# Kernel optimization log

Measured on AMD Instinct MI355X. Metric: run time of the kernel, lower is better.

The kernel has to match this reference:

```python
import jax, jax.numpy as jnp
import numpy as np

NUM_HEADS = 8
NEG_INF = -1e30


def _within_bucket_rank(idx):
    # idx: [U] int32 bucket ids; returns occurrence count of each id among earlier positions
    U = idx.shape[0]
    order = jnp.argsort(idx, stable=True)
    sv = idx[order]
    pos = jnp.arange(U, dtype=jnp.int32)
    is_start = jnp.concatenate([jnp.ones((1,), bool), sv[1:] != sv[:-1]])
    start = jax.lax.cummax(jnp.where(is_start, pos, 0))
    rank = pos - start
    return jnp.zeros(U, jnp.int32).at[order].set(rank)


def setup_inputs() -> dict:
    key = jax.random.key(0)
    ks = jax.random.split(key, 10)
    B, U, G, E = 8, 16384, 64, 128
    lin = jnp.linspace(0.0, 1.0, G)
    gx, gy = jnp.meshgrid(lin, lin, indexing='ij')
    xc_on_grid = jnp.broadcast_to(jnp.stack([gx, gy], -1), (B, G, G, 2)).astype(jnp.float32)
    s = 0.02
    return {
        'xc_off_grid': jax.random.uniform(ks[0], (B, U, 2), jnp.float32),
        'xc_on_grid': xc_on_grid,
        'zc_off_grid': jax.random.normal(ks[1], (B, U, E), jnp.float32),
        'zc_on_grid': jax.random.normal(ks[2], (B, G, G, E), jnp.float32),
        'latents': jax.random.normal(ks[3], (G * G, E), jnp.float32),
        'fake_embedding': jax.random.normal(ks[4], (E,), jnp.float32),
        'Wq': jax.random.normal(ks[5], (E, E), jnp.float32) * s,
        'Wk': jax.random.normal(ks[6], (E, E), jnp.float32) * s,
        'Wv': jax.random.normal(ks[7], (E, E), jnp.float32) * s,
        'Wo': jax.random.normal(ks[8], (E, E), jnp.float32) * s,
        'ignore_on_grid': 0,
    }


def _bucketize(xc_off_grid, xc_on_grid):
    # returns nearest flat grid index per off-grid point, shape [B, U] int32
    B = xc_off_grid.shape[0]
    dims = xc_on_grid.shape[1:-1]
    S = int(np.prod(dims))
    grid_shape = jnp.asarray(dims, jnp.float32)
    x_on = xc_on_grid.reshape(B, S, -1)
    xmin = x_on.min(axis=(0, 1))
    xmax = x_on.max(axis=(0, 1))
    spacing = (xmax - xmin) / (grid_shape - 1.0)
    nm = jnp.floor((xc_off_grid - xmin + spacing / 2) / spacing)
    nm = jnp.clip(nm, 0.0, grid_shape - 1.0)
    # strides as in the original: flip(cumprod([1, *dims])[:-1])
    strides = np.flip(np.cumprod(np.concatenate([[1], np.asarray(dims)]))[:-1]).astype(np.float32)
    return (nm * jnp.asarray(strides)).sum(-1).astype(jnp.int32)


def _mhca(latents_q, kv, valid, Wq, Wk, Wv, Wo):
    # latents_q: [N,1,E], kv: [N,P,E], valid: [N,P] bool
    N, P, E = kv.shape
    H, Dh = NUM_HEADS, E // NUM_HEADS
    q = (latents_q @ Wq).reshape(N, 1, H, Dh)
    k = (kv @ Wk).reshape(N, P, H, Dh)
    v = (kv @ Wv).reshape(N, P, H, Dh)
    scores = jnp.einsum('nqhd,nkhd->nhqk', q, k) / jnp.sqrt(jnp.asarray(Dh, q.dtype))
    scores = jnp.where(valid[:, None, None, :], scores, NEG_INF)
    attn = jax.nn.softmax(scores, axis=-1)
    out = jnp.einsum('nhqk,nkhd->nqhd', attn, v).reshape(N, 1, E)
    return out @ Wo


def reference(xc_off_grid, xc_on_grid, zc_off_grid, zc_on_grid, latents, fake_embedding, Wq, Wk, Wv, Wo, ignore_on_grid):
    B, U, E = zc_off_grid.shape
    dims = xc_on_grid.shape[1:-1]
    S = int(np.prod(dims))
    z_on = zc_on_grid.reshape(B, S, E)

    nearest_idx = _bucketize(xc_off_grid, xc_on_grid)          # [B, U]
    cumcount = jax.vmap(_within_bucket_rank)(nearest_idx)       # [B, U]
    flat_seg = (nearest_idx + jnp.arange(B, dtype=jnp.int32)[:, None] * S).reshape(-1)
    counts = jax.ops.segment_sum(jnp.ones(B * U, jnp.int32), flat_seg, num_segments=B * S)
    max_patch = int(jax.device_get(counts.max())) + 1           # +1 slot for on-grid/fake token

    # ragged scatter of off-grid tokens into padded per-bucket buffer
    grid_stacked = jnp.zeros((B * S, max_patch, E), zc_off_grid.dtype)
    grid_stacked = grid_stacked.at[flat_seg, cumcount.reshape(-1)].set(zc_off_grid.reshape(B * U, E))
    if ignore_on_grid:
        last = jnp.broadcast_to(fake_embedding, (B * S, E))
    else:
        last = z_on.reshape(B * S, E)
    grid_stacked = grid_stacked.at[:, -1].set(last)

    slot = jnp.arange(max_patch)
    valid = (slot[None, :] < counts[:, None]) | (slot[None, :] == max_patch - 1)  # [B*S, P]

    lat = jnp.broadcast_to(latents[None], (B, S, E)).reshape(B * S, 1, E)
    zc = _mhca(lat, grid_stacked, valid, Wq, Wk, Wv, Wo)        # [B*S, 1, E]
    return zc.reshape(B, *dims, E)
```

## Files before the change

kernel.cpp:

```cpp
#include <hip/hip_runtime.h>
#include <hip/hip_bf16.h>
#include <math.h>

namespace {
constexpr int B_  = 8;
constexpr int U_  = 16384;
constexpr int S_  = 4096;
constexpr int E_  = 128;
constexpr int NTOK  = B_ * U_;
constexpr int NCELL = B_ * S_;
constexpr int CAP = 32;
constexpr int SWZ2 = 2 * 16384;
constexpr int ASZ  = 128 * 1024;
}

typedef __attribute__((ext_vector_type(8))) short bf16x8;
typedef __attribute__((ext_vector_type(4))) float f32x4;

__device__ inline unsigned short bf16rne(float x) {
  unsigned u = __float_as_uint(x);
  u = u + 0x7fffu + ((u >> 16) & 1u);
  return (unsigned short)(u >> 16);
}

__device__ inline float bf16tof(unsigned short h) {
  return __uint_as_float(((unsigned)h) << 16);
}

__device__ inline bf16x8 pack8(float4 a, float4 b) {
  union { __hip_bfloat162 h; unsigned int u; } q0, q1, q2, q3;
  q0.h = __float22bfloat162_rn(make_float2(a.x, a.y));
  q1.h = __float22bfloat162_rn(make_float2(a.z, a.w));
  q2.h = __float22bfloat162_rn(make_float2(b.x, b.y));
  q3.h = __float22bfloat162_rn(make_float2(b.z, b.w));
  union { unsigned int u[4]; bf16x8 v; } r;
  r.u[0] = q0.u; r.u[1] = q1.u; r.u[2] = q2.u; r.u[3] = q3.u;
  return r.v;
}

__global__ __launch_bounds__(1024, 4) void setup_kernel(
    const float* __restrict__ Wq, const float* __restrict__ Wk,
    const float* __restrict__ Wv, const float* __restrict__ Wo,
    const float* __restrict__ xc_off,
    unsigned short* __restrict__ Wsw,
    unsigned short* __restrict__ Ahi, unsigned short* __restrict__ Alo,
    int* __restrict__ cnt, int* __restrict__ sorted) {
  const int tid = threadIdx.x;

  if (blockIdx.x < 16) {
    const int n = tid;
    const int eg = n >> 6, h = (n >> 3) & 7, el = n & 7;
    const int e = eg * 8 + el;
    const float* wk = Wk + (size_t)e * 128 + h * 16;
    float wkv[16];
#pragma unroll
    for (int j = 0; j < 16; j += 4) {
      float4 t = *(const float4*)(wk + j);
      wkv[j] = t.x; wkv[j + 1] = t.y; wkv[j + 2] = t.z; wkv[j + 3] = t.w;
    }
    union { unsigned short s[8]; uint4 v; } rh, rl;
#pragma unroll
    for (int r = 0; r < 8; ++r) {
      const int k = (blockIdx.x << 3) + r;
      const float* wq = Wq + (size_t)k * 128 + h * 16;
      float acc = 0.f;
#pragma unroll
      for (int j = 0; j < 16; j += 4) {
        float4 t = *(const float4*)(wq + j);
        acc = fmaf(t.x, wkv[j], acc);
        acc = fmaf(t.y, wkv[j + 1], acc);
        acc = fmaf(t.z, wkv[j + 2], acc);
        acc = fmaf(t.w, wkv[j + 3], acc);
      }
      acc *= 0.25f;
      const unsigned short hh = bf16rne(acc);
      rh.s[r] = hh;
      rl.s[r] = bf16rne(acc - bf16tof(hh));
    }
    const size_t fo = ((size_t)blockIdx.x * 1024 + n) * 8;
    *(uint4*)(Ahi + fo) = rh.v;
    *(uint4*)(Alo + fo) = rl.v;
  } else {
    const int base = (blockIdx.x - 16) * 1024 + tid;
    const int stride = 240 * 1024;
    for (int i = base; i < SWZ2 + NTOK; i += stride) {
      if (i < SWZ2) {
        const int w = i >> 14, e = i & 16383;
        const int k = e >> 7, n = e & 127;
        const float* src = (w == 0) ? Wv : Wo;
        Wsw[w * 16384 + (((k >> 3) * 128 + n) << 3) + (k & 7)] = bf16rne(src[e]);
      } else {
        const int tok = i - SWZ2;
        const int b = tok >> 14;
        const float sp = 1.0f / 63.0f;
        const float half = sp * 0.5f;
        const float x0 = xc_off[(size_t)tok * 2 + 0];
        const float x1 = xc_off[(size_t)tok * 2 + 1];
        float n0 = floorf((x0 - 0.0f + half) / sp);
        float n1 = floorf((x1 - 0.0f + half) / sp);
        n0 = fminf(fmaxf(n0, 0.0f), 63.0f);
        n1 = fminf(fmaxf(n1, 0.0f), 63.0f);
        const int seg = b * S_ + (int)(n0 * 64.0f + n1);
        const int rank = atomicAdd(&cnt[seg], 1);
        if (rank < CAP) sorted[seg * CAP + rank] = tok;
      }
    }
  }
}

__global__ __launch_bounds__(512, 4) void qkt_gemm(
    const float* __restrict__ latents,
    const unsigned short* __restrict__ Ahi,
    const unsigned short* __restrict__ Alo,
    unsigned short* __restrict__ QKt) {
  const int tid = threadIdx.x;
  const int wave = tid >> 6, lane = tid & 63;
  const int c = lane & 15, g = lane >> 4;
  const int rb = blockIdx.x >> 1, cb = blockIdx.x & 1;
  const int wr = wave >> 2, wc = wave & 3;
  const int t0 = rb * 32 + wr * 16;
  const int n0 = cb * 512 + wc * 128;

  f32x4 acc[8];
#pragma unroll
  for (int i = 0; i < 8; ++i) acc[i] = {0.f, 0.f, 0.f, 0.f};

  const float* arow = latents + (size_t)(t0 + c) * E_ + g * 8;
#pragma unroll
  for (int ks = 0; ks < 4; ++ks) {
    float4 a0 = *(const float4*)(arow + ks * 32);
    float4 a1 = *(const float4*)(arow + ks * 32 + 4);
    bf16x8 af = pack8(a0, a1);
    const size_t kg = (size_t)(ks * 4 + g) * 1024;
#pragma unroll
    for (int nt = 0; nt < 8; ++nt) {
      const size_t fo = (kg + n0 + nt * 16 + c) * 8;
      acc[nt] = __builtin_amdgcn_mfma_f32_16x16x32_bf16(
          af, *(const bf16x8*)(Ahi + fo), acc[nt], 0, 0, 0);
      acc[nt] = __builtin_amdgcn_mfma_f32_16x16x32_bf16(
          af, *(const bf16x8*)(Alo + fo), acc[nt], 0, 0, 0);
    }
  }
#pragma unroll
  for (int nt = 0; nt < 8; ++nt)
#pragma unroll
    for (int r = 0; r < 4; ++r)
      QKt[(size_t)(t0 + g * 4 + r) * 1024 + n0 + nt * 16 + c] = bf16rne(acc[nt][r]);
}

__global__ __launch_bounds__(512, 4) void fused_cells(
    const float* __restrict__ zc_off, const float* __restrict__ zc_on,
    const float* __restrict__ fake, const int* __restrict__ ignore_flag,
    const unsigned short* __restrict__ Wv_sw,
    const unsigned short* __restrict__ Wo_sw,
    const unsigned short* __restrict__ QKt, const int* __restrict__ cnt,
    const int* __restrict__ sorted, float* __restrict__ out) {
  __shared__ __align__(16) unsigned short wv[16384];
  __shared__ __align__(16) float wbuf[8][8][24];
  const int tid = threadIdx.x;
  {
    const uint4* sv = (const uint4*)Wv_sw;
    uint4* dv = (uint4*)wv;
#pragma unroll
    for (int i = 0; i < 4; ++i) dv[i * 512 + tid] = sv[i * 512 + tid];
  }
  const int ign = *ignore_flag;
  __syncthreads();

  const int wave = tid >> 6, lane = tid & 63;
  const int c = lane & 15, g = lane >> 4;
  const int half = c >> 3;
  const int hwr  = g >> 1;
  const bf16x8* bv = (const bf16x8*)wv;

  const int slot = blockIdx.x * 8 + wave;
  const int cA = slot * 2, cB = cA + 1;
  const int sA = cA & (S_ - 1);
  const int nA = min(cnt[cA], CAP);
  const int nB = min(cnt[cB], CAP);
  const int cH = half ? cB : cA;
  const int nH = half ? nB : nA;
  const int baseH = cH * CAP;
  const bf16x8* bqk = (const bf16x8*)(QKt + (size_t)(sA + half) * 1024);

  float num_acc[8], den_acc[8];
#pragma unroll
  for (int i = 0; i < 8; ++i) { num_acc[i] = 0.f; den_acc[i] = 0.f; }

  const int chunks = max((nA + 8) >> 3, (nB + 8) >> 3);

  for (int ch = 0; ch < chunks; ++ch) {
    const int jj = ch * 8 + (c & 7);
    const float* arow;
    if (jj < nH)       arow = zc_off + (size_t)sorted[baseH + jj] * E_;
    else if (jj == nH) arow = ign ? fake : (zc_on + (size_t)cH * E_);
    else               arow = zc_on;
    arow += g * 8;

    bf16x8 af[4];
#pragma unroll
    for (int ks = 0; ks < 4; ++ks) {
      float4 a0 = *(const float4*)(arow + ks * 32);
      float4 a1 = *(const float4*)(arow + ks * 32 + 4);
      af[ks] = pack8(a0, a1);
    }

    f32x4 aS = {0.f, 0.f, 0.f, 0.f};
#pragma unroll
    for (int ks = 0; ks < 4; ++ks)
      aS = __builtin_amdgcn_mfma_f32_16x16x32_bf16(af[ks], bqk[(ks * 4 + g) * 8 + (c & 7)], aS, 0, 0, 0);

    if (hwr == half) {
      float4 w4;
#pragma unroll
      for (int r = 0; r < 4; ++r) {
        const int t = g * 4 + r;
        const int jt = ch * 8 + (t & 7);
        ((float*)&w4)[r] = (jt <= nH) ? __expf(aS[r]) : 0.f;
      }
      *(float4*)&wbuf[wave][c & 7][g * 4] = w4;
    }

#pragma unroll 2
    for (int h = 0; h < 8; ++h) {
      const float4 wr4 = *(const float4*)&wbuf[wave][h][g * 4];

      const int bo = g * 128 + c + h * 16;
      f32x4 aV = {0.f, 0.f, 0.f, 0.f};
#pragma unroll
      for (int ks = 0; ks < 4; ++ks)
        aV = __builtin_amdgcn_mfma_f32_16x16x32_bf16(af[ks], bv[bo + ks * 512], aV, 0, 0, 0);

      float sv = 0.f, sd;
      sv = fmaf(wr4.x, aV[0], sv);
      sv = fmaf(wr4.y, aV[1], sv);
      sv = fmaf(wr4.z, aV[2], sv);
      sv = fmaf(wr4.w, aV[3], sv);
      sd = wr4.x + wr4.y + wr4.z + wr4.w;
      num_acc[h] += sv;
      den_acc[h] += sd;
    }
  }

#pragma unroll
  for (int i = 0; i < 8; ++i) {
    num_acc[i] += __shfl_xor(num_acc[i], 16, 64);
    den_acc[i] += __shfl_xor(den_acc[i], 16, 64);
  }
  const int hb = (g & 1) * 4;

  bf16x8 wof[4];
#pragma unroll
  for (int ks = 0; ks < 4; ++ks)
    wof[ks] = *(const bf16x8*)(Wo_sw +
        ((size_t)((ks * 4 + g) * 128 + wave * 16 + c)) * 8);

  __syncthreads();
  float* obuf = (float*)wv;
  const int lrow = wave * 2 + hwr;
#pragma unroll
  for (int b = 0; b < 4; ++b) {
    const int h = hb + b;
    obuf[lrow * 132 + h * 16 + c] = num_acc[h] / den_acc[h];
  }
  __syncthreads();

  const float* nrow = obuf + c * 132 + g * 8;
  f32x4 acc2 = {0.f, 0.f, 0.f, 0.f};
#pragma unroll
  for (int ks = 0; ks < 4; ++ks) {
    float4 a0 = *(const float4*)(nrow + ks * 32);
    float4 a1 = *(const float4*)(nrow + ks * 32 + 4);
    acc2 = __builtin_amdgcn_mfma_f32_16x16x32_bf16(pack8(a0, a1), wof[ks], acc2, 0, 0, 0);
  }
  const int cell0 = blockIdx.x * 16;
#pragma unroll
  for (int r = 0; r < 4; ++r)
    out[(size_t)(cell0 + g * 4 + r) * E_ + wave * 16 + c] = acc2[r];
}

extern "C" void kernel_launch(void* const* d_in, const int* in_sizes, int n_in,
                              void* d_out, int out_size, void* d_ws, size_t ws_size,
                              hipStream_t stream) {
  const float* xc_off  = (const float*)d_in[0];
  const float* zc_off  = (const float*)d_in[2];
  const float* zc_on   = (const float*)d_in[3];
  const float* latents = (const float*)d_in[4];
  const float* fake    = (const float*)d_in[5];
  const float* Wq      = (const float*)d_in[6];
  const float* Wk      = (const float*)d_in[7];
  const float* Wv      = (const float*)d_in[8];
  const float* Wo      = (const float*)d_in[9];
  const int*   ignore  = (const int*)d_in[10];

  float* out = (float*)d_out;

  unsigned short* QKt = (unsigned short*)d_ws;
  unsigned short* Wsw = QKt + (size_t)S_ * 1024;
  int* cnt    = (int*)(Wsw + SWZ2);
  int* sorted = cnt + NCELL;
  unsigned short* Ahi = (unsigned short*)(sorted + NCELL * CAP);
  unsigned short* Alo = Ahi + ASZ;
  unsigned short* Wv_sw = Wsw;
  unsigned short* Wo_sw = Wsw + 16384;

  hipMemsetAsync(cnt, 0, NCELL * sizeof(int), stream);
  setup_kernel<<<256, 1024, 0, stream>>>(Wq, Wk, Wv, Wo, xc_off,
                                         Wsw, Ahi, Alo, cnt, sorted);
  qkt_gemm<<<256, 512, 0, stream>>>(latents, Ahi, Alo, QKt);
  fused_cells<<<2048, 512, 0, stream>>>(zc_off, zc_on, fake, ignore,
                                        Wv_sw, Wo_sw, QKt, cnt, sorted, out);
}
```

Baseline: 185.2 us.

## Shrink fused_cells blocks, read Wv from global, restructure chunk loop and output GEMM

The fused cell kernel now runs 256-thread blocks with four waves instead of 512 threads, and drops the 32KB shared-memory staging of Wv, reading its fragments straight from global memory (L2/L1) so more blocks can be resident. The chunk loop is reordered so the on-grid token sits in slot 7 of the first chunk, which saves a chunk for some cell counts. The sorted index is read unconditionally, which is why the sorted buffer is now zeroed with a larger memset. The output projection computes two N-tiles per wave over a half-empty 16-row tile, which wastes half of that MFMA work. It also adds a larger memset and repeated global reads of Wv in exchange for lower LDS use and higher occupancy.

```diff
diff --git a/kernel.cpp b/kernel.cpp
--- a/kernel.cpp
+++ b/kernel.cpp
@@ -148,36 +148,31 @@
       QKt[(size_t)(t0 + g * 4 + r) * 1024 + n0 + nt * 16 + c] = bf16rne(acc[nt][r]);
 }
 
-__global__ __launch_bounds__(512, 4) void fused_cells(
+__global__ __launch_bounds__(256, 8) void fused_cells(
     const float* __restrict__ zc_off, const float* __restrict__ zc_on,
     const float* __restrict__ fake, const int* __restrict__ ignore_flag,
     const unsigned short* __restrict__ Wv_sw,
     const unsigned short* __restrict__ Wo_sw,
     const unsigned short* __restrict__ QKt, const int* __restrict__ cnt,
     const int* __restrict__ sorted, float* __restrict__ out) {
-  __shared__ __align__(16) unsigned short wv[16384];
-  __shared__ __align__(16) float wbuf[8][8][24];
+  __shared__ __align__(16) float wbuf[4][8][24];
+  __shared__ __align__(16) float obuf[16 * 132];
   const int tid = threadIdx.x;
-  {
-    const uint4* sv = (const uint4*)Wv_sw;
-    uint4* dv = (uint4*)wv;
-#pragma unroll
-    for (int i = 0; i < 4; ++i) dv[i * 512 + tid] = sv[i * 512 + tid];
-  }
+  for (int i = 8 * 132 + tid; i < 16 * 132; i += 256) obuf[i] = 0.f;
   const int ign = *ignore_flag;
-  __syncthreads();
 
   const int wave = tid >> 6, lane = tid & 63;
   const int c = lane & 15, g = lane >> 4;
   const int half = c >> 3;
   const int hwr  = g >> 1;
-  const bf16x8* bv = (const bf16x8*)wv;
-
-  const int slot = blockIdx.x * 8 + wave;
+  const bf16x8* bv = (const bf16x8*)Wv_sw;
+
+  const int slot = blockIdx.x * 4 + wave;
   const int cA = slot * 2, cB = cA + 1;
   const int sA = cA & (S_ - 1);
-  const int nA = min(cnt[cA], CAP);
-  const int nB = min(cnt[cB], CAP);
+  const int2 cc = *(const int2*)(cnt + cA);
+  const int nA = min(cc.x, CAP);
+  const int nB = min(cc.y, CAP);
   const int cH = half ? cB : cA;
   const int nH = half ? nB : nA;
   const int baseH = cH * CAP;
@@ -187,14 +182,14 @@
 #pragma unroll
   for (int i = 0; i < 8; ++i) { num_acc[i] = 0.f; den_acc[i] = 0.f; }
 
-  const int chunks = max((nA + 8) >> 3, (nB + 8) >> 3);
-
-  for (int ch = 0; ch < chunks; ++ch) {
-    const int jj = ch * 8 + (c & 7);
-    const float* arow;
-    if (jj < nH)       arow = zc_off + (size_t)sorted[baseH + jj] * E_;
-    else if (jj == nH) arow = ign ? fake : (zc_on + (size_t)cH * E_);
-    else               arow = zc_on;
+  int ch = 0;
+  do {
+    const int s = c & 7;
+    const bool isOn = (ch == 0) & (s == 7);
+    const int jj = (ch == 0) ? s : 7 + (ch - 1) * 8 + s;
+    const int sidx = sorted[baseH + (isOn ? 0 : min(jj, CAP - 1))];
+    const float* arow = isOn ? (ign ? fake : zc_on + (size_t)cH * E_)
+                             : zc_off + (size_t)sidx * E_;
     arow += g * 8;
 
     bf16x8 af[4];
@@ -214,9 +209,10 @@
       float4 w4;
 #pragma unroll
       for (int r = 0; r < 4; ++r) {
-        const int t = g * 4 + r;
-        const int jt = ch * 8 + (t & 7);
-        ((float*)&w4)[r] = (jt <= nH) ? __expf(aS[r]) : 0.f;
+        const int sl = (g * 4 + r) & 7;
+        const bool von = (ch == 0) & (sl == 7);
+        const int tj = (ch == 0) ? sl : 7 + (ch - 1) * 8 + sl;
+        ((float*)&w4)[r] = (von | (tj < nH)) ? __expf(aS[r]) : 0.f;
       }
       *(float4*)&wbuf[wave][c & 7][g * 4] = w4;
     }
@@ -240,7 +236,7 @@
       num_acc[h] += sv;
       den_acc[h] += sd;
     }
-  }
+  } while (++ch < 1 + (max(nA, nB) >> 3));
 
 #pragma unroll
   for (int i = 0; i < 8; ++i) {
@@ -249,34 +245,40 @@
   }
   const int hb = (g & 1) * 4;
 
-  bf16x8 wof[4];
-#pragma unroll
-  for (int ks = 0; ks < 4; ++ks)
-    wof[ks] = *(const bf16x8*)(Wo_sw +
-        ((size_t)((ks * 4 + g) * 128 + wave * 16 + c)) * 8);
-
-  __syncthreads();
-  float* obuf = (float*)wv;
   const int lrow = wave * 2 + hwr;
 #pragma unroll
   for (int b = 0; b < 4; ++b) {
     const int h = hb + b;
     obuf[lrow * 132 + h * 16 + c] = num_acc[h] / den_acc[h];
   }
+  bf16x8 wof[2][4];
+#pragma unroll
+  for (int nt = 0; nt < 2; ++nt)
+#pragma unroll
+    for (int ks = 0; ks < 4; ++ks)
+      wof[nt][ks] = *(const bf16x8*)(Wo_sw +
+          ((size_t)((ks * 4 + g) * 128 + wave * 32 + nt * 16 + c)) * 8);
   __syncthreads();
 
   const float* nrow = obuf + c * 132 + g * 8;
-  f32x4 acc2 = {0.f, 0.f, 0.f, 0.f};
+  f32x4 acc2[2] = {{0.f, 0.f, 0.f, 0.f}, {0.f, 0.f, 0.f, 0.f}};
 #pragma unroll
   for (int ks = 0; ks < 4; ++ks) {
     float4 a0 = *(const float4*)(nrow + ks * 32);
     float4 a1 = *(const float4*)(nrow + ks * 32 + 4);
-    acc2 = __builtin_amdgcn_mfma_f32_16x16x32_bf16(pack8(a0, a1), wof[ks], acc2, 0, 0, 0);
-  }
-  const int cell0 = blockIdx.x * 16;
-#pragma unroll
-  for (int r = 0; r < 4; ++r)
-    out[(size_t)(cell0 + g * 4 + r) * E_ + wave * 16 + c] = acc2[r];
+    const bf16x8 af = pack8(a0, a1);
+#pragma unroll
+    for (int nt = 0; nt < 2; ++nt)
+      acc2[nt] = __builtin_amdgcn_mfma_f32_16x16x32_bf16(af, wof[nt][ks], acc2[nt], 0, 0, 0);
+  }
+  const int cell0 = blockIdx.x * 8;
+  if (hwr == 0) {
+#pragma unroll
+    for (int nt = 0; nt < 2; ++nt)
+#pragma unroll
+      for (int r = 0; r < 4; ++r)
+        out[(size_t)(cell0 + g * 4 + r) * E_ + wave * 32 + nt * 16 + c] = acc2[nt][r];
+  }
 }
 
 extern "C" void kernel_launch(void* const* d_in, const int* in_sizes, int n_in,
@@ -304,10 +306,10 @@
   unsigned short* Wv_sw = Wsw;
   unsigned short* Wo_sw = Wsw + 16384;
 
-  hipMemsetAsync(cnt, 0, NCELL * sizeof(int), stream);
+  hipMemsetAsync(cnt, 0, NCELL * sizeof(int) * (1 + CAP), stream);
   setup_kernel<<<256, 1024, 0, stream>>>(Wq, Wk, Wv, Wo, xc_off,
                                          Wsw, Ahi, Alo, cnt, sorted);
   qkt_gemm<<<256, 512, 0, stream>>>(latents, Ahi, Alo, QKt);
-  fused_cells<<<2048, 512, 0, stream>>>(zc_off, zc_on, fake, ignore,
+  fused_cells<<<4096, 256, 0, stream>>>(zc_off, zc_on, fake, ignore,
                                         Wv_sw, Wo_sw, QKt, cnt, sorted, out);
 }
```

New measurement: 255.5 us. 38.0% more time.

## Software-pipeline token row loads and hoist QK fragments into registers

Applied to the files above, without the earlier changes.

The fused cell kernel now prefetches the next chunk of token rows into registers while computing the current one. The first token load is issued before the shared-memory Wv copy and barrier, and the QK^T fragments are held in registers instead of being reloaded every chunk. Token slots are reordered so the on-grid token sits in slot 7 of the first chunk, and out-of-range slots read a clamped sorted index. Because that clamped read can touch unwritten entries, the memset is widened to also zero the sorted index buffer. This adds register pressure and a larger memset.

```diff
diff --git a/kernel.cpp b/kernel.cpp
--- a/kernel.cpp
+++ b/kernel.cpp
@@ -158,65 +158,82 @@
   __shared__ __align__(16) unsigned short wv[16384];
   __shared__ __align__(16) float wbuf[8][8][24];
   const int tid = threadIdx.x;
-  {
-    const uint4* sv = (const uint4*)Wv_sw;
-    uint4* dv = (uint4*)wv;
-#pragma unroll
-    for (int i = 0; i < 4; ++i) dv[i * 512 + tid] = sv[i * 512 + tid];
-  }
-  const int ign = *ignore_flag;
-  __syncthreads();
-
   const int wave = tid >> 6, lane = tid & 63;
   const int c = lane & 15, g = lane >> 4;
   const int half = c >> 3;
   const int hwr  = g >> 1;
-  const bf16x8* bv = (const bf16x8*)wv;
 
   const int slot = blockIdx.x * 8 + wave;
   const int cA = slot * 2, cB = cA + 1;
   const int sA = cA & (S_ - 1);
-  const int nA = min(cnt[cA], CAP);
-  const int nB = min(cnt[cB], CAP);
   const int cH = half ? cB : cA;
+  const int baseH = cH * CAP;
+
+  const int2 cc = *(const int2*)(cnt + cA);
+  const int ign = *ignore_flag;
+
+  bf16x8 bq[4];
+  {
+    const bf16x8* bqk = (const bf16x8*)(QKt + (size_t)(sA + half) * 1024);
+#pragma unroll
+    for (int ks = 0; ks < 4; ++ks) bq[ks] = bqk[(ks * 4 + g) * 8 + (c & 7)];
+  }
+
+  float4 f4[8];
+  auto zload = [&](int ch) {
+    const int s = c & 7;
+    const bool isOn = (ch == 0) & (s == 7);
+    const int jj = (ch == 0) ? s : 7 + (ch - 1) * 8 + s;
+    const int sidx = sorted[baseH + (isOn ? 0 : min(jj, CAP - 1))];
+    const float* arow = isOn ? (ign ? fake : zc_on + (size_t)cH * E_)
+                             : zc_off + (size_t)sidx * E_;
+    arow += g * 8;
+#pragma unroll
+    for (int ks = 0; ks < 4; ++ks) {
+      f4[2 * ks]     = *(const float4*)(arow + ks * 32);
+      f4[2 * ks + 1] = *(const float4*)(arow + ks * 32 + 4);
+    }
+  };
+  zload(0);
+
+  {
+    const uint4* sv = (const uint4*)Wv_sw;
+    uint4* dv = (uint4*)wv;
+#pragma unroll
+    for (int i = 0; i < 4; ++i) dv[i * 512 + tid] = sv[i * 512 + tid];
+  }
+  __syncthreads();
+  const bf16x8* bv = (const bf16x8*)wv;
+
+  const int nA = min(cc.x, CAP);
+  const int nB = min(cc.y, CAP);
   const int nH = half ? nB : nA;
-  const int baseH = cH * CAP;
-  const bf16x8* bqk = (const bf16x8*)(QKt + (size_t)(sA + half) * 1024);
+  const int nch = 1 + (max(nA, nB) >> 3);
 
   float num_acc[8], den_acc[8];
 #pragma unroll
   for (int i = 0; i < 8; ++i) { num_acc[i] = 0.f; den_acc[i] = 0.f; }
 
-  const int chunks = max((nA + 8) >> 3, (nB + 8) >> 3);
-
-  for (int ch = 0; ch < chunks; ++ch) {
-    const int jj = ch * 8 + (c & 7);
-    const float* arow;
-    if (jj < nH)       arow = zc_off + (size_t)sorted[baseH + jj] * E_;
-    else if (jj == nH) arow = ign ? fake : (zc_on + (size_t)cH * E_);
-    else               arow = zc_on;
-    arow += g * 8;
-
+  int ch = 0;
+  do {
     bf16x8 af[4];
 #pragma unroll
-    for (int ks = 0; ks < 4; ++ks) {
-      float4 a0 = *(const float4*)(arow + ks * 32);
-      float4 a1 = *(const float4*)(arow + ks * 32 + 4);
-      af[ks] = pack8(a0, a1);
-    }
+    for (int ks = 0; ks < 4; ++ks) af[ks] = pack8(f4[2 * ks], f4[2 * ks + 1]);
+    if (ch + 1 < nch) zload(ch + 1);
 
     f32x4 aS = {0.f, 0.f, 0.f, 0.f};
 #pragma unroll
     for (int ks = 0; ks < 4; ++ks)
-      aS = __builtin_amdgcn_mfma_f32_16x16x32_bf16(af[ks], bqk[(ks * 4 + g) * 8 + (c & 7)], aS, 0, 0, 0);
+      aS = __builtin_amdgcn_mfma_f32_16x16x32_bf16(af[ks], bq[ks], aS, 0, 0, 0);
 
     if (hwr == half) {
       float4 w4;
 #pragma unroll
       for (int r = 0; r < 4; ++r) {
-        const int t = g * 4 + r;
-        const int jt = ch * 8 + (t & 7);
-        ((float*)&w4)[r] = (jt <= nH) ? __expf(aS[r]) : 0.f;
+        const int sl = (g * 4 + r) & 7;
+        const bool von = (ch == 0) & (sl == 7);
+        const int tj = (ch == 0) ? sl : 7 + (ch - 1) * 8 + sl;
+        ((float*)&w4)[r] = (von | (tj < nH)) ? __expf(aS[r]) : 0.f;
       }
       *(float4*)&wbuf[wave][c & 7][g * 4] = w4;
     }
@@ -240,7 +257,7 @@
       num_acc[h] += sv;
       den_acc[h] += sd;
     }
-  }
+  } while (++ch < nch);
 
 #pragma unroll
   for (int i = 0; i < 8; ++i) {
@@ -304,7 +321,7 @@
   unsigned short* Wv_sw = Wsw;
   unsigned short* Wo_sw = Wsw + 16384;
 
-  hipMemsetAsync(cnt, 0, NCELL * sizeof(int), stream);
+  hipMemsetAsync(cnt, 0, NCELL * sizeof(int) * (1 + CAP), stream);
   setup_kernel<<<256, 1024, 0, stream>>>(Wq, Wk, Wv, Wo, xc_off,
                                          Wsw, Ahi, Alo, cnt, sorted);
   qkt_gemm<<<256, 512, 0, stream>>>(latents, Ahi, Alo, QKt);
```

After: 188.1 us. About the same (+1.6%).

## Restructure pre-pass kernels: fold memset into prep, merge QK^T GEMM with bucketing

Applied to the files above, without the earlier changes.

The memset of the bucket counters moves into a small prep kernel that also builds the split-bf16 Wq·Wk^T factors. The QK^T GEMM is merged with the Wv/Wo swizzle and the bucketing atomics into a single mid kernel whose blocks split the two jobs. The GEMM now keeps its B fragments in registers across eight row tiles. The cell kernel also loads its two counts as one int2 and raises wave priority around the MFMA section. The goal is fewer launches, letting bucketing overlap the GEMM, at the cost of fewer blocks for the bucketing atomics and the GEMM.

```diff
diff --git a/kernel.cpp b/kernel.cpp
--- a/kernel.cpp
+++ b/kernel.cpp
@@ -38,15 +38,11 @@
   return r.v;
 }
 
-__global__ __launch_bounds__(1024, 4) void setup_kernel(
+__global__ __launch_bounds__(1024, 4) void prep_kernel(
     const float* __restrict__ Wq, const float* __restrict__ Wk,
-    const float* __restrict__ Wv, const float* __restrict__ Wo,
-    const float* __restrict__ xc_off,
-    unsigned short* __restrict__ Wsw,
     unsigned short* __restrict__ Ahi, unsigned short* __restrict__ Alo,
-    int* __restrict__ cnt, int* __restrict__ sorted) {
+    int* __restrict__ cnt) {
   const int tid = threadIdx.x;
-
   if (blockIdx.x < 16) {
     const int n = tid;
     const int eg = n >> 6, h = (n >> 3) & 7, el = n & 7;
@@ -81,8 +77,64 @@
     *(uint4*)(Ahi + fo) = rh.v;
     *(uint4*)(Alo + fo) = rl.v;
   } else {
-    const int base = (blockIdx.x - 16) * 1024 + tid;
-    const int stride = 240 * 1024;
+    cnt[(blockIdx.x - 16) * 1024 + tid] = 0;
+  }
+}
+
+__global__ __launch_bounds__(512, 1) void mid_kernel(
+    const float* __restrict__ latents,
+    const unsigned short* __restrict__ Ahi,
+    const unsigned short* __restrict__ Alo,
+    unsigned short* __restrict__ QKt,
+    const float* __restrict__ Wv, const float* __restrict__ Wo,
+    const float* __restrict__ xc_off,
+    unsigned short* __restrict__ Wsw,
+    int* __restrict__ cnt, int* __restrict__ sorted) {
+  const int tid = threadIdx.x;
+
+  if (blockIdx.x < 128) {
+    const int wave = tid >> 6, lane = tid & 63;
+    const int c = lane & 15, g = lane >> 4;
+    const int rb = blockIdx.x >> 2;
+    const int cbg = blockIdx.x & 3;
+    const int n0 = cbg * 256 + wave * 32;
+
+    bf16x8 bhi[4][2], blo[4][2];
+#pragma unroll
+    for (int ks = 0; ks < 4; ++ks) {
+      const size_t kg = (size_t)(ks * 4 + g) * 1024;
+#pragma unroll
+      for (int nt = 0; nt < 2; ++nt) {
+        const size_t fo = (kg + n0 + nt * 16 + c) * 8;
+        bhi[ks][nt] = *(const bf16x8*)(Ahi + fo);
+        blo[ks][nt] = *(const bf16x8*)(Alo + fo);
+      }
+    }
+
+    for (int rt = 0; rt < 8; ++rt) {
+      const int t0 = rb * 128 + rt * 16;
+      f32x4 acc[2] = {{0.f, 0.f, 0.f, 0.f}, {0.f, 0.f, 0.f, 0.f}};
+      const float* arow = latents + (size_t)(t0 + c) * E_ + g * 8;
+#pragma unroll
+      for (int ks = 0; ks < 4; ++ks) {
+        float4 a0 = *(const float4*)(arow + ks * 32);
+        float4 a1 = *(const float4*)(arow + ks * 32 + 4);
+        const bf16x8 af = pack8(a0, a1);
+#pragma unroll
+        for (int nt = 0; nt < 2; ++nt) {
+          acc[nt] = __builtin_amdgcn_mfma_f32_16x16x32_bf16(af, bhi[ks][nt], acc[nt], 0, 0, 0);
+          acc[nt] = __builtin_amdgcn_mfma_f32_16x16x32_bf16(af, blo[ks][nt], acc[nt], 0, 0, 0);
+        }
+      }
+#pragma unroll
+      for (int nt = 0; nt < 2; ++nt)
+#pragma unroll
+        for (int r = 0; r < 4; ++r)
+          QKt[(size_t)(t0 + g * 4 + r) * 1024 + n0 + nt * 16 + c] = bf16rne(acc[nt][r]);
+    }
+  } else {
+    const int base = (blockIdx.x - 128) * 512 + tid;
+    const int stride = 128 * 512;
     for (int i = base; i < SWZ2 + NTOK; i += stride) {
       if (i < SWZ2) {
         const int w = i >> 14, e = i & 16383;
@@ -108,46 +160,6 @@
   }
 }
 
-__global__ __launch_bounds__(512, 4) void qkt_gemm(
-    const float* __restrict__ latents,
-    const unsigned short* __restrict__ Ahi,
-    const unsigned short* __restrict__ Alo,
-    unsigned short* __restrict__ QKt) {
-  const int tid = threadIdx.x;
-  const int wave = tid >> 6, lane = tid & 63;
-  const int c = lane & 15, g = lane >> 4;
-  const int rb = blockIdx.x >> 1, cb = blockIdx.x & 1;
-  const int wr = wave >> 2, wc = wave & 3;
-  const int t0 = rb * 32 + wr * 16;
-  const int n0 = cb * 512 + wc * 128;
-
-  f32x4 acc[8];
-#pragma unroll
-  for (int i = 0; i < 8; ++i) acc[i] = {0.f, 0.f, 0.f, 0.f};
-
-  const float* arow = latents + (size_t)(t0 + c) * E_ + g * 8;
-#pragma unroll
-  for (int ks = 0; ks < 4; ++ks) {
-    float4 a0 = *(const float4*)(arow + ks * 32);
-    float4 a1 = *(const float4*)(arow + ks * 32 + 4);
-    bf16x8 af = pack8(a0, a1);
-    const size_t kg = (size_t)(ks * 4 + g) * 1024;
-#pragma unroll
-    for (int nt = 0; nt < 8; ++nt) {
-      const size_t fo = (kg + n0 + nt * 16 + c) * 8;
-      acc[nt] = __builtin_amdgcn_mfma_f32_16x16x32_bf16(
-          af, *(const bf16x8*)(Ahi + fo), acc[nt], 0, 0, 0);
-      acc[nt] = __builtin_amdgcn_mfma_f32_16x16x32_bf16(
-          af, *(const bf16x8*)(Alo + fo), acc[nt], 0, 0, 0);
-    }
-  }
-#pragma unroll
-  for (int nt = 0; nt < 8; ++nt)
-#pragma unroll
-    for (int r = 0; r < 4; ++r)
-      QKt[(size_t)(t0 + g * 4 + r) * 1024 + n0 + nt * 16 + c] = bf16rne(acc[nt][r]);
-}
-
 __global__ __launch_bounds__(512, 4) void fused_cells(
     const float* __restrict__ zc_off, const float* __restrict__ zc_on,
     const float* __restrict__ fake, const int* __restrict__ ignore_flag,
@@ -176,8 +188,9 @@
   const int slot = blockIdx.x * 8 + wave;
   const int cA = slot * 2, cB = cA + 1;
   const int sA = cA & (S_ - 1);
-  const int nA = min(cnt[cA], CAP);
-  const int nB = min(cnt[cB], CAP);
+  const int2 cc = *(const int2*)(cnt + cA);
+  const int nA = min(cc.x, CAP);
+  const int nB = min(cc.y, CAP);
   const int cH = half ? cB : cA;
   const int nH = half ? nB : nA;
   const int baseH = cH * CAP;
@@ -205,6 +218,8 @@
       af[ks] = pack8(a0, a1);
     }
 
+    __builtin_amdgcn_s_setprio(1);
+
     f32x4 aS = {0.f, 0.f, 0.f, 0.f};
 #pragma unroll
     for (int ks = 0; ks < 4; ++ks)
@@ -214,9 +229,9 @@
       float4 w4;
 #pragma unroll
       for (int r = 0; r < 4; ++r) {
-        const int t = g * 4 + r;
-        const int jt = ch * 8 + (t & 7);
-        ((float*)&w4)[r] = (jt <= nH) ? __expf(aS[r]) : 0.f;
+        const int sl = (g * 4 + r) & 7;
+        const int tj = ch * 8 + sl;
+        ((float*)&w4)[r] = (tj <= nH) ? __expf(aS[r]) : 0.f;
       }
       *(float4*)&wbuf[wave][c & 7][g * 4] = w4;
     }
@@ -240,6 +255,8 @@
       num_acc[h] += sv;
       den_acc[h] += sd;
     }
+
+    __builtin_amdgcn_s_setprio(0);
   }
 
 #pragma unroll
@@ -304,10 +321,9 @@
   unsigned short* Wv_sw = Wsw;
   unsigned short* Wo_sw = Wsw + 16384;
 
-  hipMemsetAsync(cnt, 0, NCELL * sizeof(int), stream);
-  setup_kernel<<<256, 1024, 0, stream>>>(Wq, Wk, Wv, Wo, xc_off,
-                                         Wsw, Ahi, Alo, cnt, sorted);
-  qkt_gemm<<<256, 512, 0, stream>>>(latents, Ahi, Alo, QKt);
+  prep_kernel<<<48, 1024, 0, stream>>>(Wq, Wk, Ahi, Alo, cnt);
+  mid_kernel<<<256, 512, 0, stream>>>(latents, Ahi, Alo, QKt,
+                                      Wv, Wo, xc_off, Wsw, cnt, sorted);
   fused_cells<<<2048, 512, 0, stream>>>(zc_off, zc_on, fake, ignore,
                                         Wv_sw, Wo_sw, QKt, cnt, sorted, out);
 }
```

Result: faster. 180.8 us (-2.4%).
